# Optimization experiments

Measured on AMD Instinct MI355X. Metric: run time of the kernel, lower is better.

The kernel has to match this reference:

```python
import jax, jax.numpy as jnp
import numpy as np

IGNORE_LABEL = 255
THRESH = 0.9
MIN_KEPT = 10000


def setup_inputs() -> dict:
    key = jax.random.key(0)
    k1, k2 = jax.random.split(key)
    n, c, d, h, w = 2, 12, 64, 128, 128
    predict = jax.random.normal(k1, (n, c, d, h, w), dtype=jnp.float32)
    target = jax.random.randint(k2, (n, d, h, w), 0, c, dtype=jnp.int64)
    return {"predict": predict, "target": target}


def reference(predict, target):
    n, c, d, h, w = predict.shape
    # rollaxis(predict, 1).reshape(c, -1): class-major flattening, matching target.ravel()
    logits = jnp.moveaxis(predict, 1, 0).reshape(c, -1)          # (c, N)
    labels = target.reshape(-1)                                   # (N,)
    valid = labels != IGNORE_LABEL
    safe_lab = jnp.where(valid, labels, 0)

    logp = jax.nn.log_softmax(logits, axis=0)                     # (c, N), stable softmax
    lp_at_label = jnp.take_along_axis(logp, safe_lab[None, :], axis=0)[0]  # (N,)
    prob_at_label = jnp.exp(lp_at_label)                          # softmax prob of true class

    num_valid = valid.sum()
    # k-th smallest true-class prob among valid pixels (invalid -> +inf pushed to end)
    sorted_prob = jnp.sort(jnp.where(valid, prob_at_label, jnp.inf))
    k_idx = jnp.maximum(jnp.minimum(MIN_KEPT, num_valid) - 1, 0)
    th_val = sorted_prob[k_idx]
    threshold = jnp.maximum(th_val, THRESH)

    # if min_kept >= num_valid: keep all valid; else keep hard examples (prob <= threshold)
    keep_all = MIN_KEPT >= num_valid
    kept = valid & jnp.where(keep_all, True, prob_at_label <= threshold)

    # masked mean cross-entropy (CrossEntropyLoss with ignore_index, mean reduction)
    nll = -lp_at_label
    num = jnp.sum(jnp.where(kept, nll, 0.0))
    cnt = jnp.sum(kept)
    loss = num / jnp.maximum(cnt, 1).astype(nll.dtype)
    return loss
```

## Files before the change

kernel.cpp:

```cpp
#include <hip/hip_runtime.h>
#include <hip/hip_bf16.h>
#include <math.h>


#define IGNORE_LABEL 255
#define MIN_KEPT 10000u

constexpr int   C         = 12;
constexpr int   PIX_SHIFT = 20;
constexpr int   PIX_MASK  = (1 << PIX_SHIFT) - 1;
constexpr int   NBINS     = 2048;
constexpr float BIN_SCALE = (float)NBINS / 0.1f;

struct Ws {
    double       sum_p3;
    unsigned int cnt_p3;
    unsigned int flag;
    float        threshold;
    unsigned int done;
    unsigned int done2;
    unsigned int pad[9];
    unsigned int hist[NBINS];
};

__device__ inline float wave_reduce_f(float v) {
    #pragma unroll
    for (int o = 32; o > 0; o >>= 1) v += __shfl_down(v, o, 64);
    return v;
}
__device__ inline unsigned int wave_reduce_u(unsigned int v) {
    #pragma unroll
    for (int o = 32; o > 0; o >>= 1) v += __shfl_down(v, o, 64);
    return v;
}
__device__ inline double wave_reduce_d(double v) {
    #pragma unroll
    for (int o = 32; o > 0; o >>= 1) v += __shfl_down(v, o, 64);
    return v;
}

__global__ __launch_bounds__(256, 4) void main_pass_kernel(
        const float* __restrict__ pred, const int* __restrict__ tgt,
        Ws* __restrict__ ws, uint4* __restrict__ partials, int npix) {
    const int tid = blockIdx.x * blockDim.x + threadIdx.x;

    float        my_sle = 0.0f, my_sva = 0.0f;
    unsigned int my_cle = 0u,   my_cva = 0u;

    const int p0 = tid << 3;
    if (p0 < npix) {
        const float* base = pred +
            (((size_t)(p0 >> PIX_SHIFT) * C) << PIX_SHIFT) + (p0 & PIX_MASK);
        const int4 la = *(const int4*)(tgt + p0);
        const int4 lb = *(const int4*)(tgt + p0 + 4);
        const int lab[8] = {la.x, la.y, la.z, la.w, lb.x, lb.y, lb.z, lb.w};

        float E[8]  = {0,0,0,0,0,0,0,0};
        float ll[8] = {0,0,0,0,0,0,0,0};
        #pragma unroll
        for (int ci = 0; ci < C; ++ci) {
            const float* csrc = base + ((size_t)ci << PIX_SHIFT);
            const float4 v0 = *(const float4*)(csrc);
            const float4 v1 = *(const float4*)(csrc + 4);
            const float vv[8] = {v0.x, v0.y, v0.z, v0.w, v1.x, v1.y, v1.z, v1.w};
            #pragma unroll
            for (int j = 0; j < 8; ++j) {
                E[j] += __expf(vv[j]);
                if (lab[j] == ci) ll[j] = vv[j];
            }
        }
        #pragma unroll
        for (int j = 0; j < 8; ++j) {
            const float ls   = __logf(E[j]);
            const float nll  = ls - ll[j];
            const float prob = __expf(ll[j] - ls);
            if (lab[j] != IGNORE_LABEL) {
                my_cva += 1u;
                my_sva += nll;
                if (prob <= 0.9f) {
                    my_cle += 1u;
                    my_sle += nll;
                } else {
                    int b = (int)((prob - 0.9f) * BIN_SCALE);
                    b = b < 0 ? 0 : (b >= NBINS - 1 ? NBINS - 1 : b);
                    atomicAdd(&ws->hist[b], 1u);
                }
            }
        }
    }

    __shared__ float        s_le[4], s_va[4];
    __shared__ unsigned int s_cle[4], s_cva[4];
    const int wid = threadIdx.x >> 6, lane = threadIdx.x & 63;
    const float        r_le = wave_reduce_f(my_sle);
    const float        r_va = wave_reduce_f(my_sva);
    const unsigned int r_cl = wave_reduce_u(my_cle);
    const unsigned int r_cv = wave_reduce_u(my_cva);
    if (lane == 0) { s_le[wid] = r_le; s_va[wid] = r_va; s_cle[wid] = r_cl; s_cva[wid] = r_cv; }
    __syncthreads();
    if (threadIdx.x == 0) {
        uint4 p;
        p.x = __float_as_uint(s_le[0] + s_le[1] + s_le[2] + s_le[3]);
        p.y = __float_as_uint(s_va[0] + s_va[1] + s_va[2] + s_va[3]);
        p.z = s_cle[0] + s_cle[1] + s_cle[2] + s_cle[3];
        p.w = s_cva[0] + s_cva[1] + s_cva[2] + s_cva[3];
        partials[blockIdx.x] = p;
    }
}

__global__ __launch_bounds__(1024) void reduce_finalize_kernel(
        Ws* __restrict__ ws, const uint4* __restrict__ partials,
        int nblocks, float* __restrict__ out) {
    double       sle = 0.0, sva = 0.0;
    unsigned int cle = 0u,  cva = 0u;
    for (int i = threadIdx.x; i < nblocks; i += 1024) {
        const uint4 p = partials[i];
        sle += (double)__uint_as_float(p.x);
        sva += (double)__uint_as_float(p.y);
        cle += p.z;
        cva += p.w;
    }
    __shared__ double       d_le[16], d_va[16];
    __shared__ unsigned int u_le[16], u_va[16];
    const int wid = threadIdx.x >> 6, lane = threadIdx.x & 63;
    const double       r_sle = wave_reduce_d(sle);
    const double       r_sva = wave_reduce_d(sva);
    const unsigned int r_cle = wave_reduce_u(cle);
    const unsigned int r_cva = wave_reduce_u(cva);
    if (lane == 0) { d_le[wid] = r_sle; d_va[wid] = r_sva; u_le[wid] = r_cle; u_va[wid] = r_cva; }
    __syncthreads();
    if (threadIdx.x == 0) {
        double       t_sle = 0.0, t_sva = 0.0;
        unsigned int t_cle = 0u,  t_cva = 0u;
        #pragma unroll
        for (int i = 0; i < 16; ++i) {
            t_sle += d_le[i]; t_sva += d_va[i]; t_cle += u_le[i]; t_cva += u_va[i];
        }
        const unsigned int nv = t_cva;
        const unsigned int k  = nv < MIN_KEPT ? nv : MIN_KEPT;
        if (MIN_KEPT >= nv) {
            out[0] = (float)(t_sva / (double)(nv > 0u ? nv : 1u));
            ws->flag = 0u;
        } else if (t_cle >= k) {
            out[0] = (float)(t_sle / (double)(t_cle > 0u ? t_cle : 1u));
            ws->flag = 0u;
        } else {
            unsigned int cum = t_cle;
            int b = NBINS - 1;
            for (int i = 0; i < NBINS; ++i) {
                cum += ws->hist[i];
                if (cum >= k) { b = i; break; }
            }
            ws->threshold = 0.9f + (float)(b + 1) * (0.1f / (float)NBINS);
            ws->flag = 1u;
            out[0] = 0.0f;
        }
    }
}

__global__ __launch_bounds__(256) void fallback_kernel(
        const float* __restrict__ pred, const int* __restrict__ tgt,
        Ws* __restrict__ ws, float* __restrict__ out, int npix_q) {
    if (ws->flag == 0u) return;
    const float th = ws->threshold;
    const int stride = gridDim.x * blockDim.x;

    float        my_s = 0.0f;
    unsigned int my_c = 0u;
    for (int t = blockIdx.x * blockDim.x + threadIdx.x; t < npix_q; t += stride) {
        const int p0 = t << 2;
        const float* base = pred +
            (((size_t)(p0 >> PIX_SHIFT) * C) << PIX_SHIFT) + (p0 & PIX_MASK);
        const int4 li = *(const int4*)(tgt + p0);
        const int lab[4] = {li.x, li.y, li.z, li.w};
        float s[4] = {0,0,0,0}, l_lab[4] = {0,0,0,0};
        #pragma unroll
        for (int ci = 0; ci < C; ++ci) {
            const float4 v = *(const float4*)(base + ((size_t)ci << PIX_SHIFT));
            const float vv[4] = {v.x, v.y, v.z, v.w};
            #pragma unroll
            for (int j = 0; j < 4; ++j) {
                s[j] += __expf(vv[j]);
                if (lab[j] == ci) l_lab[j] = vv[j];
            }
        }
        #pragma unroll
        for (int j = 0; j < 4; ++j) {
            const float ls   = __logf(s[j]);
            const float nll  = ls - l_lab[j];
            const float prob = __expf(l_lab[j] - ls);
            if (lab[j] != IGNORE_LABEL && prob <= th) { my_c += 1u; my_s += nll; }
        }
    }
    __shared__ float        s_s[4];
    __shared__ unsigned int s_c[4];
    const int wid = threadIdx.x >> 6, lane = threadIdx.x & 63;
    const float        r_s = wave_reduce_f(my_s);
    const unsigned int r_c = wave_reduce_u(my_c);
    if (lane == 0) { s_s[wid] = r_s; s_c[wid] = r_c; }
    __syncthreads();
    if (threadIdx.x == 0) {
        const float        t_s = s_s[0] + s_s[1] + s_s[2] + s_s[3];
        const unsigned int t_c = s_c[0] + s_c[1] + s_c[2] + s_c[3];
        if (t_s != 0.0f) atomicAdd(&ws->sum_p3, (double)t_s);
        if (t_c)         atomicAdd(&ws->cnt_p3, t_c);
        __threadfence();
        const unsigned int prev = atomicAdd(&ws->done2, 1u);
        if (prev == gridDim.x - 1u) {
            const unsigned int cnt = ws->cnt_p3;
            out[0] = (float)(ws->sum_p3 / (double)(cnt > 0u ? cnt : 1u));
        }
    }
}

extern "C" void kernel_launch(void* const* d_in, const int* in_sizes, int n_in,
                              void* d_out, int out_size, void* d_ws, size_t ws_size,
                              hipStream_t stream) {
    const float* pred = (const float*)d_in[0];
    const int*   tgt  = (const int*)d_in[1];
    float*       out  = (float*)d_out;
    Ws*          ws   = (Ws*)d_ws;
    uint4*       partials = (uint4*)((char*)d_ws + sizeof(Ws));

    const int npix   = in_sizes[1];
    const int npix_q = npix >> 2;
    const int blocks = (npix / 8 + 255) / 256;

    hipMemsetAsync(d_ws, 0, sizeof(Ws), stream);
    main_pass_kernel<<<blocks, 256, 0, stream>>>(pred, tgt, ws, partials, npix);
    reduce_finalize_kernel<<<1, 1024, 0, stream>>>(ws, partials, blocks, out);
    fallback_kernel<<<128, 256, 0, stream>>>(pred, tgt, ws, out, npix_q);
}
```

Baseline: 158.4 us.

## Stage logits through LDS with async global_load_lds in two class phases

The main pass now copies each block's 2048-pixel tile of logits into shared memory using the direct global-to-LDS load builtin, six classes at a time in two phases, and then reads them back as float4 for the softmax and NLL work. Each thread now reads contiguous 1024-pixel halves instead of 8 consecutive pixels, and the launch bound drops to 3 blocks per CU to fit the 48 KB LDS buffer. The goal is better coalesced, asynchronous HBM streaming for this bandwidth-bound pass, at the cost of extra barriers and LDS traffic. Occupancy is lower, and loads are not overlapped across phases.

```diff
diff --git a/kernel.cpp b/kernel.cpp
--- a/kernel.cpp
+++ b/kernel.cpp
@@ -39,72 +39,99 @@
     return v;
 }
 
-__global__ __launch_bounds__(256, 4) void main_pass_kernel(
+__device__ inline void stage16(const float* g, float* l) {
+    __builtin_amdgcn_global_load_lds(
+        (const __attribute__((address_space(1))) void*)g,
+        (__attribute__((address_space(3))) void*)l,
+        16, 0, 0);
+}
+
+__global__ __launch_bounds__(256, 3) void main_pass_kernel(
         const float* __restrict__ pred, const int* __restrict__ tgt,
         Ws* __restrict__ ws, uint4* __restrict__ partials, int npix) {
-    const int tid = blockIdx.x * blockDim.x + threadIdx.x;
-
-    float        my_sle = 0.0f, my_sva = 0.0f;
-    unsigned int my_cle = 0u,   my_cva = 0u;
-
-    const int p0 = tid << 3;
-    if (p0 < npix) {
-        const float* base = pred +
-            (((size_t)(p0 >> PIX_SHIFT) * C) << PIX_SHIFT) + (p0 & PIX_MASK);
-        const int4 la = *(const int4*)(tgt + p0);
-        const int4 lb = *(const int4*)(tgt + p0 + 4);
-        const int lab[8] = {la.x, la.y, la.z, la.w, lb.x, lb.y, lb.z, lb.w};
-
-        float E[8]  = {0,0,0,0,0,0,0,0};
-        float ll[8] = {0,0,0,0,0,0,0,0};
-        #pragma unroll
-        for (int ci = 0; ci < C; ++ci) {
-            const float* csrc = base + ((size_t)ci << PIX_SHIFT);
-            const float4 v0 = *(const float4*)(csrc);
-            const float4 v1 = *(const float4*)(csrc + 4);
+    __shared__ float smem[6 * 2048];
+
+    const int blk   = blockIdx.x;
+    const int t     = threadIdx.x;
+    const int wave  = t >> 6, lane = t & 63;
+    const int bpix0 = blk << 11;
+    if (bpix0 >= npix) return;
+
+    const size_t sbase = (((size_t)(bpix0 >> PIX_SHIFT) * C) << PIX_SHIFT)
+                       + (size_t)(bpix0 & PIX_MASK);
+
+    const int4 la = *(const int4*)(tgt + bpix0 + (t << 2));
+    const int4 lb = *(const int4*)(tgt + bpix0 + 1024 + (t << 2));
+    const int lab[8] = {la.x, la.y, la.z, la.w, lb.x, lb.y, lb.z, lb.w};
+
+    float E[8]  = {0,0,0,0,0,0,0,0};
+    float ll[8] = {0,0,0,0,0,0,0,0};
+
+    const float* gw = pred + sbase + (wave << 9) + (lane << 2);
+
+    #pragma unroll
+    for (int ph = 0; ph < 2; ++ph) {
+        #pragma unroll
+        for (int ci = 0; ci < 6; ++ci) {
+            const int c = ph * 6 + ci;
+            const float* g0 = gw + ((size_t)c << PIX_SHIFT);
+            float* l0 = smem + (ci << 11) + (wave << 9);
+            stage16(g0,       l0);
+            stage16(g0 + 256, l0 + 256);
+        }
+        __syncthreads();
+
+        #pragma unroll
+        for (int ci = 0; ci < 6; ++ci) {
+            const int c = ph * 6 + ci;
+            const float4 v0 = *(const float4*)(smem + (ci << 11) + (t << 2));
+            const float4 v1 = *(const float4*)(smem + (ci << 11) + 1024 + (t << 2));
             const float vv[8] = {v0.x, v0.y, v0.z, v0.w, v1.x, v1.y, v1.z, v1.w};
             #pragma unroll
             for (int j = 0; j < 8; ++j) {
                 E[j] += __expf(vv[j]);
-                if (lab[j] == ci) ll[j] = vv[j];
-            }
-        }
-        #pragma unroll
-        for (int j = 0; j < 8; ++j) {
-            const float ls   = __logf(E[j]);
-            const float nll  = ls - ll[j];
-            const float prob = __expf(ll[j] - ls);
-            if (lab[j] != IGNORE_LABEL) {
-                my_cva += 1u;
-                my_sva += nll;
-                if (prob <= 0.9f) {
-                    my_cle += 1u;
-                    my_sle += nll;
-                } else {
-                    int b = (int)((prob - 0.9f) * BIN_SCALE);
-                    b = b < 0 ? 0 : (b >= NBINS - 1 ? NBINS - 1 : b);
-                    atomicAdd(&ws->hist[b], 1u);
-                }
+                if (lab[j] == c) ll[j] = vv[j];
+            }
+        }
+        __syncthreads();
+    }
+
+    float        my_sle = 0.0f, my_sva = 0.0f;
+    unsigned int my_cle = 0u,   my_cva = 0u;
+    #pragma unroll
+    for (int j = 0; j < 8; ++j) {
+        const float ls   = __logf(E[j]);
+        const float nll  = ls - ll[j];
+        const float prob = __expf(ll[j] - ls);
+        if (lab[j] != IGNORE_LABEL) {
+            my_cva += 1u;
+            my_sva += nll;
+            if (prob <= 0.9f) {
+                my_cle += 1u;
+                my_sle += nll;
+            } else {
+                int b = (int)((prob - 0.9f) * BIN_SCALE);
+                b = b < 0 ? 0 : (b >= NBINS - 1 ? NBINS - 1 : b);
+                atomicAdd(&ws->hist[b], 1u);
             }
         }
     }
 
     __shared__ float        s_le[4], s_va[4];
     __shared__ unsigned int s_cle[4], s_cva[4];
-    const int wid = threadIdx.x >> 6, lane = threadIdx.x & 63;
     const float        r_le = wave_reduce_f(my_sle);
     const float        r_va = wave_reduce_f(my_sva);
     const unsigned int r_cl = wave_reduce_u(my_cle);
     const unsigned int r_cv = wave_reduce_u(my_cva);
-    if (lane == 0) { s_le[wid] = r_le; s_va[wid] = r_va; s_cle[wid] = r_cl; s_cva[wid] = r_cv; }
+    if (lane == 0) { s_le[wave] = r_le; s_va[wave] = r_va; s_cle[wave] = r_cl; s_cva[wave] = r_cv; }
     __syncthreads();
-    if (threadIdx.x == 0) {
+    if (t == 0) {
         uint4 p;
         p.x = __float_as_uint(s_le[0] + s_le[1] + s_le[2] + s_le[3]);
         p.y = __float_as_uint(s_va[0] + s_va[1] + s_va[2] + s_va[3]);
         p.z = s_cle[0] + s_cle[1] + s_cle[2] + s_cle[3];
         p.w = s_cva[0] + s_cva[1] + s_cva[2] + s_cva[3];
-        partials[blockIdx.x] = p;
+        partials[blk] = p;
     }
 }
 
@@ -224,7 +251,7 @@
 
     const int npix   = in_sizes[1];
     const int npix_q = npix >> 2;
-    const int blocks = (npix / 8 + 255) / 256;
+    const int blocks = (npix + 2047) / 2048;
 
     hipMemsetAsync(d_ws, 0, sizeof(Ws), stream);
     main_pass_kernel<<<blocks, 256, 0, stream>>>(pred, tgt, ws, partials, npix);
```

Measured after the change: 161.8 us. 1.02x slower.
